# Kernel tuning notes

Hardware: AMD Instinct MI355X
Metric: run time of the kernel (lower is better)

## Reference

```python
import math
import jax, jax.numpy as jnp
import numpy as np

STRIDE = 8
IMG = 2048
NA = 9            # num anchors per cell (len(cfg['anchor_size']))
NC = 80           # num classes
TOPK = 1000
CONF = 0.05
NMS_T = 0.6
CTR_CLAMP = 32.0
EXP_CLAMP = math.log(1e8)            # DEFAULT_EXP_CLAMP
SCALE_CLAMP = math.log(1000.0 / 16)  # DEFAULT_SCALE_CLAMP


def setup_inputs() -> dict:
    key = jax.random.key(0)
    k1, k2, k3 = jax.random.split(key, 3)
    H = W = IMG // STRIDE  # 256
    obj_pred = jax.random.normal(k1, (1, NA, H, W), jnp.float32)
    cls_pred = jax.random.normal(k2, (1, NA * NC, H, W), jnp.float32)
    reg_pred = jax.random.normal(k3, (1, NA * 4, H, W), jnp.float32) * 0.5
    # generate_anchors: grid centers (+0.5)*stride, tiled anchor sizes -> [H*W*NA, 4] (cx,cy,w,h)
    ys, xs = jnp.meshgrid(jnp.arange(H), jnp.arange(W), indexing='ij')
    xy = (jnp.stack([xs, ys], -1).reshape(-1, 2).astype(jnp.float32) + 0.5) * STRIDE
    sizes = jnp.array([[32, 32], [64, 64], [128, 128], [32, 64], [64, 128],
                       [128, 256], [64, 32], [128, 64], [256, 128]], jnp.float32)
    anchor_boxes = jnp.concatenate(
        [jnp.repeat(xy[:, None, :], NA, axis=1),
         jnp.broadcast_to(sizes[None], (H * W, NA, 2))], axis=-1).reshape(-1, 4)
    return {"obj_pred": obj_pred, "cls_pred": cls_pred,
            "reg_pred": reg_pred, "anchor_boxes": anchor_boxes}


def _detect(obj_pred, cls_pred, reg_pred, anchor_boxes):
    B, _, H, W = obj_pred.shape
    obj = obj_pred.reshape(B, NA, 1, H, W)
    cls = cls_pred.reshape(B, NA, NC, H, W)
    # normalized_cls_pred = cls + obj - log(1 + exp(clamp(cls)) + exp(clamp(obj)))
    norm = cls + obj - jnp.log(1.0 + jnp.exp(jnp.minimum(cls, EXP_CLAMP))
                               + jnp.exp(jnp.minimum(obj, EXP_CLAMP)))
    norm = norm.transpose(0, 3, 4, 1, 2).reshape(B, -1, NC)[0]          # [M, NC]
    reg = reg_pred.reshape(B, NA, 4, H, W).transpose(0, 3, 4, 1, 2).reshape(B, -1, 4)[0]  # [M, 4]
    prob = jax.nn.sigmoid(norm)
    scores_all = prob.max(axis=-1)
    labels_all = prob.argmax(axis=-1)
    scores, idx = jax.lax.top_k(scores_all, TOPK)                        # descending
    labels = labels_all[idx]
    reg = reg[idx]
    anc = anchor_boxes[idx]
    # decode_boxes
    ctr_off = jnp.clip(reg[..., :2] * anc[..., 2:], -CTR_CLAMP, CTR_CLAMP)
    ctr = anc[..., :2] + ctr_off
    wh = anc[..., 2:] * jnp.exp(jnp.minimum(reg[..., 2:], SCALE_CLAMP))
    boxes = jnp.concatenate([ctr - 0.5 * wh, ctr + 0.5 * wh], axis=-1)
    boxes = jnp.clip(boxes / IMG, 0.0, 1.0)
    return scores, labels, boxes


def _nms_keep(scores, labels, boxes):
    # scores are sorted descending; per-class greedy NMS == class-masked global greedy NMS
    valid = scores >= CONF
    x1, y1, x2, y2 = boxes[:, 0], boxes[:, 1], boxes[:, 2], boxes[:, 3]
    areas = (x2 - x1) * (y2 - y1)
    xx1 = jnp.maximum(x1[:, None], x1[None, :])
    yy1 = jnp.maximum(y1[:, None], y1[None, :])
    xx2 = jnp.minimum(x2[:, None], x2[None, :])
    yy2 = jnp.minimum(y2[:, None], y2[None, :])
    inter = jnp.maximum(1e-28, xx2 - xx1) * jnp.maximum(1e-28, yy2 - yy1)
    iou = inter / (areas[:, None] + areas[None, :] - inter + 1e-14)      # [N, N]
    sup = (iou > NMS_T) & (labels[:, None] == labels[None, :])
    later = jnp.arange(TOPK)[None, :] > jnp.arange(TOPK)[:, None]

    def body(i, keep):
        row = sup[i] & later[i] & keep[i]   # i suppresses only if still kept
        return keep & ~row

    return jax.lax.fori_loop(0, TOPK, body, valid)


def reference(obj_pred, cls_pred, reg_pred, anchor_boxes):
    scores, labels, boxes = _detect(obj_pred, cls_pred, reg_pred, anchor_boxes)
    keep = _nms_keep(scores, labels, boxes)
    # fixed-shape outputs: detections sorted by score with a keep mask
    return scores, labels, boxes, keep
```

## Files before the change

kernel.cpp:

```cpp
#include <hip/hip_runtime.h>
#include <stdint.h>

#define NA 9
#define NC 80
#define NTOT 589824
#define NT4  147456
#define TOPK 1000
#define CONF 0.05f
#define NMS_T 0.6
#define CTR_CLAMP 32.0
#define IMGF 2048.0
#define SCALE_CLAMP 4.135166556742356

#define BITS_OFF   0u
#define LABELS_OFF 2359296u
#define HIST_OFF   4718592u
#define CNT_OFF    4784128u
#define BARC_OFF   4784384u
#define FLAG_OFF   4792576u
#define INITF_OFF  4800768u
#define CAND_OFF   4802816u
#define BOXES_OFF  4835584u
#define LABS_OFF   4851584u
#define SUPB_OFF   4855584u

#define NBLK 512
#define SPIN_CAP 200000
#define INIT_MAGIC 0x9E3779B97F4A7C15ull

__device__ __forceinline__ void stg32(unsigned* p, unsigned v) {
  __hip_atomic_store(p, v, __ATOMIC_RELAXED, __HIP_MEMORY_SCOPE_AGENT);
}
__device__ __forceinline__ unsigned ldg32(const unsigned* p) {
  return __hip_atomic_load((unsigned*)p, __ATOMIC_RELAXED, __HIP_MEMORY_SCOPE_AGENT);
}
__device__ __forceinline__ void stg64(unsigned long long* p, unsigned long long v) {
  __hip_atomic_store(p, v, __ATOMIC_RELAXED, __HIP_MEMORY_SCOPE_AGENT);
}
__device__ __forceinline__ unsigned long long ldg64(const unsigned long long* p) {
  return __hip_atomic_load((unsigned long long*)p, __ATOMIC_RELAXED,
                           __HIP_MEMORY_SCOPE_AGENT);
}

__device__ __forceinline__ unsigned* lslot(unsigned* base, int idx) {
  return (unsigned*)((char*)base + (size_t)idx * 256u);
}

__device__ __forceinline__ void barrier_sync(unsigned* cnts, unsigned* flags,
                                             int b, int bid, unsigned target,
                                             bool i_arrive) {
  __syncthreads();
  if (threadIdx.x == 0) {
    if (i_arrive)
      __hip_atomic_fetch_add(lslot(cnts, b * 8 + (bid & 7)), 1u, __ATOMIC_RELAXED,
                             __HIP_MEMORY_SCOPE_AGENT);
    if (bid == 0) {
      for (int it = 0; it < SPIN_CAP; it++) {
        unsigned s = 0;
#pragma unroll
        for (int i = 0; i < 8; i++)
          s += __hip_atomic_load(lslot(cnts, b * 8 + i), __ATOMIC_RELAXED,
                                 __HIP_MEMORY_SCOPE_AGENT);
        if (s >= target) break;
        __builtin_amdgcn_s_sleep(2);
      }
#pragma unroll
      for (int i = 0; i < 8; i++)
        __hip_atomic_store(lslot(flags, b * 8 + i), 1u, __ATOMIC_RELAXED,
                           __HIP_MEMORY_SCOPE_AGENT);
    } else {
      for (int it = 0; it < SPIN_CAP; it++) {
        if (__hip_atomic_load(lslot(flags, b * 8 + (bid & 7)), __ATOMIC_RELAXED,
                              __HIP_MEMORY_SCOPE_AGENT) != 0u)
          break;
        __builtin_amdgcn_s_sleep(2);
      }
    }
  }
  __syncthreads();
  asm volatile("" ::: "memory");
}

__device__ __forceinline__ float cexpf(float x) {
#pragma clang fp contract(off)
  float m = floorf(__builtin_fmaf(x, 1.44269504088896341f, 0.5f));
  float r = __builtin_fmaf(m, -0.693359375f, x);
  r = __builtin_fmaf(m, 2.12194440e-4f, r);
  float r2 = r * r;
  float y = 1.9875691500E-4f;
  y = __builtin_fmaf(y, r, 1.3981999507E-3f);
  y = __builtin_fmaf(y, r, 8.3334519073E-3f);
  y = __builtin_fmaf(y, r, 4.1665795894E-2f);
  y = __builtin_fmaf(y, r, 1.6666665459E-1f);
  y = __builtin_fmaf(y, r, 5.0000001201E-1f);
  y = __builtin_fmaf(y, r2, r) + 1.0f;
  return ldexpf(y, (int)m);
}

__device__ __forceinline__ float clogf_(float xin) {
#pragma clang fp contract(off)
  unsigned b = __float_as_uint(xin);
  int e = (int)(b >> 23) - 126;
  float m = __uint_as_float((b & 0x007FFFFFu) | 0x3F000000u);
  if (m < 0.707106781186547524f) { e -= 1; m = m + m; }
  float x = m - 1.0f;
  float z = x * x;
  float y = 7.0376836292E-2f;
  y = __builtin_fmaf(y, x, -1.1514610310E-1f);
  y = __builtin_fmaf(y, x, 1.1676998740E-1f);
  y = __builtin_fmaf(y, x, -1.2420140846E-1f);
  y = __builtin_fmaf(y, x, 1.4249322787E-1f);
  y = __builtin_fmaf(y, x, -1.6668057665E-1f);
  y = __builtin_fmaf(y, x, 2.0000714765E-1f);
  y = __builtin_fmaf(y, x, -2.4999993993E-1f);
  y = __builtin_fmaf(y, x, 3.3333331174E-1f);
  y = y * x * z;
  float ef = (float)e;
  y = __builtin_fmaf(ef, -2.12194440e-4f, y);
  y = __builtin_fmaf(-0.5f, z, y);
  float res = x + y;
  res = __builtin_fmaf(ef, 0.693359375f, res);
  return res;
}

__device__ __forceinline__ unsigned long long shflxor64(unsigned long long v, int m) {
  unsigned lo = __shfl_xor((unsigned)v, m, 64);
  unsigned hi = __shfl_xor((unsigned)(v >> 32), m, 64);
  return ((unsigned long long)hi << 32) | lo;
}

__global__ __launch_bounds__(256) void k_fused(
    const float4* __restrict__ obj4, const float4* __restrict__ cls4,
    unsigned* __restrict__ bits_all, int* __restrict__ labels_all,
    unsigned* __restrict__ hist, const float* __restrict__ reg_pred,
    const float* __restrict__ anchors, unsigned* __restrict__ cand_cnt,
    unsigned* __restrict__ barc, unsigned* __restrict__ flags,
    unsigned* __restrict__ initf, unsigned long long* __restrict__ cand,
    float* __restrict__ out, float* __restrict__ boxes_s,
    int* __restrict__ labels_s, unsigned long long* __restrict__ supB) {
  int tid = threadIdx.x;
  int bid = blockIdx.x;

  __shared__ __align__(16) unsigned lh[16384];

  for (int i = tid; i < 16384; i += 256) lh[i] = 0u;
  if (bid == 0) {
    for (int i = tid; i < 16384; i += 256) stg32(&hist[i], 0u);
    if (tid == 0) stg32(cand_cnt, 0u);
    if (tid < 32) {
      stg32(lslot(barc, tid), 0u);
      stg32(lslot(flags, tid), 0u);
    }
  }
  __syncthreads();
  if (bid == 0 && tid < 8)
    stg64((unsigned long long*)lslot(initf, tid), INIT_MAGIC);

  {
#pragma clang fp contract(off)
    for (unsigned t4 = (unsigned)bid * 256u + (unsigned)tid; t4 < (unsigned)NT4;
         t4 += (unsigned)(NBLK * 256)) {
      int a = (int)(t4 >> 14);
      int rem = (int)(t4 & 16383u);
      float4 ov = obj4[t4];
      float ob[4] = {ov.x, ov.y, ov.z, ov.w};
      float best[4] = {-1e30f, -1e30f, -1e30f, -1e30f};
      int bc[4] = {0, 0, 0, 0};
      const float4* cp = cls4 + a * 80 * 16384 + rem;
#pragma unroll 8
      for (int c = 0; c < 80; c++) {
        float4 cv = cp[c * 16384];
        float cl[4] = {cv.x, cv.y, cv.z, cv.w};
#pragma unroll
        for (int k = 0; k < 4; k++) {
          if (cl[k] > best[k]) { best[k] = cl[k]; bc[k] = c; }
        }
      }
      unsigned bv[4];
#pragma unroll
      for (int k = 0; k < 4; k++) {
        float c = best[k], o = ob[k];
        float ec = cexpf(c);
        float eo = cexpf(o);
        float L = clogf_((1.0f + ec) + eo);
        float nrm = (c + o) - L;
        float p = 1.0f / (1.0f + cexpf(-nrm));
        bv[k] = __float_as_uint(p);
        atomicAdd(&lh[bv[k] >> 16], 1u);
      }
      unsigned po = (unsigned)(a * 65536 + rem * 4);
      stg64((unsigned long long*)&bits_all[po],
            (unsigned long long)bv[0] | ((unsigned long long)bv[1] << 32));
      stg64((unsigned long long*)&bits_all[po + 2],
            (unsigned long long)bv[2] | ((unsigned long long)bv[3] << 32));
      stg64((unsigned long long*)&labels_all[po],
            (unsigned long long)(unsigned)bc[0] |
                ((unsigned long long)(unsigned)bc[1] << 32));
      stg64((unsigned long long*)&labels_all[po + 2],
            (unsigned long long)(unsigned)bc[2] |
                ((unsigned long long)(unsigned)bc[3] << 32));
    }
  }
  __syncthreads();
  if (tid == 0) {
    for (int it = 0; it < SPIN_CAP; it++) {
      if (ldg64((unsigned long long*)lslot(initf, bid & 7)) == INIT_MAGIC) break;
      __builtin_amdgcn_s_sleep(2);
    }
  }
  __syncthreads();
  for (int b = tid; b < 16384; b += 256) {
    unsigned v = lh[b];
    if (v) atomicAdd(&hist[b], v);
  }
  barrier_sync(barc, flags, 0, bid, NBLK, true);

  unsigned cB;
  {
    unsigned base = (unsigned)tid * 64u;
    unsigned s = 0;
#pragma unroll 8
    for (int b = 0; b < 64; b++) s += hist[base + b];
    unsigned v = s;
    lh[tid] = v;
    __syncthreads();
    for (int off = 1; off < 256; off <<= 1) {
      unsigned add = (tid + off < 256) ? lh[tid + off] : 0u;
      __syncthreads();
      v += add;
      lh[tid] = v;
      __syncthreads();
    }
    unsigned nxt = (tid < 255) ? lh[tid + 1] : 0u;
    if (v >= TOPK && nxt < TOPK) { lh[260] = (unsigned)tid; lh[261] = nxt; }
    __syncthreads();
    unsigned C = lh[260];
    unsigned above = lh[261];
    if (tid < 64) {
      unsigned h = hist[C * 64u + (unsigned)tid];
      unsigned acc = h;
      for (int off = 1; off < 64; off <<= 1) {
        unsigned o = __shfl_down(acc, off, 64);
        if (tid + off < 64) acc += o;
      }
      acc += above;
      if (acc >= TOPK && (tid == 63 || (acc - h) < TOPK))
        lh[262] = C * 64u + (unsigned)tid;
    }
    __syncthreads();
    cB = lh[262];
  }

  for (unsigned t = (unsigned)bid * 256u + (unsigned)tid; t < (unsigned)NTOT;
       t += (unsigned)(NBLK * 256)) {
    unsigned bits = bits_all[t];
    bool win = (bits >> 16) >= cB;
    unsigned long long m = __ballot(win);
    if (m != 0ull) {
      int lane = tid & 63;
      int leader = __ffsll((long long)m) - 1;
      unsigned base2 = 0;
      if (lane == leader) base2 = atomicAdd(cand_cnt, (unsigned)__popcll(m));
      base2 = __shfl(base2, leader, 64);
      if (win) {
        unsigned a = t >> 16;
        unsigned hw = t & 65535u;
        unsigned j = hw * 9u + a;
        unsigned pos = base2 + (unsigned)__popcll(m & ((1ull << lane) - 1ull));
        if (pos < 4096u)
          stg64(&cand[pos], ((unsigned long long)bits << 20) |
                                (unsigned long long)(0xFFFFFu - j));
      }
    }
  }
  barrier_sync(barc, flags, 1, bid, NBLK, true);

  if (bid < 16) {
    unsigned long long* s_key = (unsigned long long*)lh;
    int c = bid * 256 + tid;
    unsigned M = ldg32(cand_cnt);
    if (M > 4096u) M = 4096u;
    unsigned long long mykey = (c < (int)M) ? ldg64(&cand[c]) : 0ull;
    unsigned rank = 0;
    int ntile = (int)((M + 255u) >> 8);
    for (int tile = 0; tile < ntile; tile++) {
      __syncthreads();
      int src = tile * 256 + tid;
      s_key[tid] = (src < (int)M) ? ldg64(&cand[src]) : 0ull;
      __syncthreads();
#pragma unroll 8
      for (int q = 0; q < 256; q++) rank += (s_key[q] > mykey) ? 1u : 0u;
    }
    if (c < (int)M && rank < TOPK) {
      int r = (int)rank;
      unsigned j = 0xFFFFFu - (unsigned)(mykey & 0xFFFFFull);
      unsigned hw = j / 9u;
      unsigned a = j - hw * 9u;
      int lab = labels_all[a * 65536u + hw];
      unsigned base = a * 4u * 65536u + hw;
      double r0 = (double)reg_pred[base];
      double r1 = (double)reg_pred[base + 65536u];
      double r2 = (double)reg_pred[base + 131072u];
      double r3 = (double)reg_pred[base + 196608u];
      double ax = (double)anchors[j * 4u + 0], ay = (double)anchors[j * 4u + 1];
      double aw = (double)anchors[j * 4u + 2], ah = (double)anchors[j * 4u + 3];
      double ox = fmin(fmax(r0 * aw, -CTR_CLAMP), CTR_CLAMP);
      double oy = fmin(fmax(r1 * ah, -CTR_CLAMP), CTR_CLAMP);
      double cx = ax + ox, cy = ay + oy;
      double ww = aw * exp(fmin(r2, SCALE_CLAMP));
      double hh = ah * exp(fmin(r3, SCALE_CLAMP));
      float x1 = (float)fmin(fmax((cx - 0.5 * ww) * (1.0 / IMGF), 0.0), 1.0);
      float y1 = (float)fmin(fmax((cy - 0.5 * hh) * (1.0 / IMGF), 0.0), 1.0);
      float x2 = (float)fmin(fmax((cx + 0.5 * ww) * (1.0 / IMGF), 0.0), 1.0);
      float y2 = (float)fmin(fmax((cy + 0.5 * hh) * (1.0 / IMGF), 0.0), 1.0);
      out[1000 + r] = (float)lab;
      out[2000 + 4 * r + 0] = x1;
      out[2000 + 4 * r + 1] = y1;
      out[2000 + 4 * r + 2] = x2;
      out[2000 + 4 * r + 3] = y2;
      stg32((unsigned*)&out[r], (unsigned)(mykey >> 20));
      stg32((unsigned*)&boxes_s[4 * r + 0], __float_as_uint(x1));
      stg32((unsigned*)&boxes_s[4 * r + 1], __float_as_uint(y1));
      stg32((unsigned*)&boxes_s[4 * r + 2], __float_as_uint(x2));
      stg32((unsigned*)&boxes_s[4 * r + 3], __float_as_uint(y2));
      stg32((unsigned*)&labels_s[r], (unsigned)lab);
    }
  }
  barrier_sync(barc, flags, 2, bid, 16, bid < 16);

  {
    float* s_bx = (float*)lh;
    int* s_lb = (int*)((char*)lh + 16000);
    for (int t = tid; t < 4000; t += 256)
      s_bx[t] = __uint_as_float(ldg32((const unsigned*)&boxes_s[t]));
    for (int t = tid; t < 1000; t += 256)
      s_lb[t] = (int)ldg32((const unsigned*)&labels_s[t]);
    __syncthreads();
    for (int half = 0; half < 2; half++) {
      int i = bid + half * NBLK;
      if (i < TOPK) {
        double ix1 = (double)s_bx[4 * i], iy1 = (double)s_bx[4 * i + 1];
        double ix2 = (double)s_bx[4 * i + 2], iy2 = (double)s_bx[4 * i + 3];
        double ia = (ix2 - ix1) * (iy2 - iy1);
        int il = s_lb[i];
        for (int rep = 0; rep < 4; rep++) {
          int j = rep * 256 + tid;
          bool s = false;
          if (j < TOPK && j > i && s_lb[j] == il) {
            double jx1 = (double)s_bx[4 * j], jy1 = (double)s_bx[4 * j + 1];
            double jx2 = (double)s_bx[4 * j + 2], jy2 = (double)s_bx[4 * j + 3];
            double xx1 = fmax(ix1, jx1), yy1 = fmax(iy1, jy1);
            double xx2 = fmin(ix2, jx2), yy2 = fmin(iy2, jy2);
            double inter = fmax(1e-28, xx2 - xx1) * fmax(1e-28, yy2 - yy1);
            double ja = (jx2 - jx1) * (jy2 - jy1);
            double iou = inter / (ia + ja - inter + 1e-14);
            s = iou > NMS_T;
          }
          unsigned long long w = __ballot(s);
          if ((tid & 63) == 0)
            stg64(&supB[(rep * 4 + (tid >> 6)) * 1024 + i], w);
        }
      }
    }
  }
  __syncthreads();
  if (tid == 0)
    __hip_atomic_fetch_add(lslot(barc, 3 * 8 + (bid & 7)), 1u, __ATOMIC_RELAXED,
                           __HIP_MEMORY_SCOPE_AGENT);
  if (bid != 0) return;
  if (tid == 0) {
    for (int it = 0; it < SPIN_CAP; it++) {
      unsigned s = 0;
#pragma unroll
      for (int i = 0; i < 8; i++)
        s += __hip_atomic_load(lslot(barc, 3 * 8 + i), __ATOMIC_RELAXED,
                               __HIP_MEMORY_SCOPE_AGENT);
      if (s >= NBLK) break;
      __builtin_amdgcn_s_sleep(2);
    }
  }
  __syncthreads();
  asm volatile("" ::: "memory");

  if (tid < 64) {
    int lane = tid;
    float* keep_out = out + 6000;
    unsigned long long inval[16];
#pragma unroll
    for (int m = 0; m < 16; m++) {
      int j = m * 64 + lane;
      bool bad = (j >= TOPK) ||
                 (__uint_as_float(ldg32((const unsigned*)&out[j])) < CONF);
      inval[m] = __ballot(bad);
    }
    unsigned long long kept[16];
#pragma unroll
    for (int b = 0; b < 16; b++) {
      unsigned long long acc = 0ull;
#pragma unroll
      for (int m = 0; m < b; m++) {
        unsigned long long r = ldg64(&supB[b * 1024 + m * 64 + lane]);
        if ((kept[m] >> lane) & 1ull) acc |= r;
      }
      if (b > 0) {
#pragma unroll
        for (int s = 1; s < 64; s <<= 1) acc |= shflxor64(acc, s);
      }
      unsigned alo = __builtin_amdgcn_readfirstlane((unsigned)acc);
      unsigned ahi = __builtin_amdgcn_readfirstlane((unsigned)(acc >> 32));
      unsigned long long cur = inval[b] | (((unsigned long long)ahi << 32) | alo);
      unsigned long long diag = ldg64(&supB[b * 1024 + b * 64 + lane]);
      unsigned dlo = (unsigned)diag, dhi = (unsigned)(diag >> 32);
#pragma unroll 8
      for (int k = 0; k < 64; k++) {
        unsigned rlo = __builtin_amdgcn_readlane(dlo, k);
        unsigned rhi = __builtin_amdgcn_readlane(dhi, k);
        unsigned long long rk = ((unsigned long long)rhi << 32) | rlo;
        unsigned long long take = ((cur >> k) & 1ull) ? 0ull : rk;
        cur |= take;
      }
      kept[b] = ~cur;
    }
#pragma unroll
    for (int m = 0; m < 16; m++) {
      int j = m * 64 + lane;
      if (j < TOPK) keep_out[j] = ((kept[m] >> lane) & 1ull) ? 1.0f : 0.0f;
    }
  }
}

extern "C" void kernel_launch(void* const* d_in, const int* in_sizes, int n_in,
                              void* d_out, int out_size, void* d_ws, size_t ws_size,
                              hipStream_t stream) {
  const float* obj = (const float*)d_in[0];
  const float* cls = (const float*)d_in[1];
  const float* reg = (const float*)d_in[2];
  const float* anc = (const float*)d_in[3];
  float* out = (float*)d_out;
  char* ws = (char*)d_ws;

  const float4* obj4 = (const float4*)obj;
  const float4* cls4 = (const float4*)cls;
  unsigned* bits_all = (unsigned*)(ws + BITS_OFF);
  int* labels_all = (int*)(ws + LABELS_OFF);
  unsigned* hist = (unsigned*)(ws + HIST_OFF);
  unsigned* cand_cnt = (unsigned*)(ws + CNT_OFF);
  unsigned* barc = (unsigned*)(ws + BARC_OFF);
  unsigned* flags = (unsigned*)(ws + FLAG_OFF);
  unsigned* initf = (unsigned*)(ws + INITF_OFF);
  unsigned long long* cand = (unsigned long long*)(ws + CAND_OFF);
  float* boxes_s = (float*)(ws + BOXES_OFF);
  int* labels_s = (int*)(ws + LABS_OFF);
  unsigned long long* supB = (unsigned long long*)(ws + SUPB_OFF);

  void* kargs[] = {(void*)&obj4,     (void*)&cls4,     (void*)&bits_all,
                   (void*)&labels_all, (void*)&hist,   (void*)&reg,
                   (void*)&anc,      (void*)&cand_cnt, (void*)&barc,
                   (void*)&flags,    (void*)&initf,    (void*)&cand,
                   (void*)&out,      (void*)&boxes_s,  (void*)&labels_s,
                   (void*)&supB};
  hipLaunchCooperativeKernel((const void*)k_fused, dim3(NBLK), dim3(256), kargs, 0,
                             stream);
}
```

Baseline: 393.2 us.

## Keep per-anchor scores in registers across grid barrier; pack label into candidate key

Each thread now scores a fixed set of float4 groups (288 per block, with 8 lanes per wave taking one extra) and keeps the probabilities and labels in registers across the histogram barrier. Candidate selection then reads from registers instead of re-reading a global bits array. The class label is packed into the low bits of the 64-bit candidate key, which removes the global labels_all array and its gather during box decode. This cuts about 4.7 MB of global writes and reads, at the cost of more live registers and uneven work where a few lanes per wave do a second scoring pass.

```diff
diff --git a/kernel.cpp b/kernel.cpp
--- a/kernel.cpp
+++ b/kernel.cpp
@@ -12,8 +12,6 @@
 #define IMGF 2048.0
 #define SCALE_CLAMP 4.135166556742356
 
-#define BITS_OFF   0u
-#define LABELS_OFF 2359296u
 #define HIST_OFF   4718592u
 #define CNT_OFF    4784128u
 #define BARC_OFF   4784384u
@@ -25,6 +23,7 @@
 #define SUPB_OFF   4855584u
 
 #define NBLK 512
+#define PER_BLK 288
 #define SPIN_CAP 200000
 #define INIT_MAGIC 0x9E3779B97F4A7C15ull
 
@@ -129,9 +128,42 @@
   return ((unsigned long long)hi << 32) | lo;
 }
 
+__device__ __forceinline__ void score4(const float4* __restrict__ obj4,
+                                       const float4* __restrict__ cls4,
+                                       unsigned t4, unsigned bv[4], int bc[4],
+                                       unsigned* lh) {
+#pragma clang fp contract(off)
+  int a = (int)(t4 >> 14);
+  int rem = (int)(t4 & 16383u);
+  float4 ov = obj4[t4];
+  float ob[4] = {ov.x, ov.y, ov.z, ov.w};
+  float best[4] = {-1e30f, -1e30f, -1e30f, -1e30f};
+  bc[0] = bc[1] = bc[2] = bc[3] = 0;
+  const float4* cp = cls4 + a * 80 * 16384 + rem;
+#pragma unroll 8
+  for (int c = 0; c < 80; c++) {
+    float4 cv = cp[c * 16384];
+    float cl[4] = {cv.x, cv.y, cv.z, cv.w};
+#pragma unroll
+    for (int k = 0; k < 4; k++) {
+      if (cl[k] > best[k]) { best[k] = cl[k]; bc[k] = c; }
+    }
+  }
+#pragma unroll
+  for (int k = 0; k < 4; k++) {
+    float c = best[k], o = ob[k];
+    float ec = cexpf(c);
+    float eo = cexpf(o);
+    float L = clogf_((1.0f + ec) + eo);
+    float nrm = (c + o) - L;
+    float p = 1.0f / (1.0f + cexpf(-nrm));
+    bv[k] = __float_as_uint(p);
+    atomicAdd(&lh[bv[k] >> 16], 1u);
+  }
+}
+
 __global__ __launch_bounds__(256) void k_fused(
     const float4* __restrict__ obj4, const float4* __restrict__ cls4,
-    unsigned* __restrict__ bits_all, int* __restrict__ labels_all,
     unsigned* __restrict__ hist, const float* __restrict__ reg_pred,
     const float* __restrict__ anchors, unsigned* __restrict__ cand_cnt,
     unsigned* __restrict__ barc, unsigned* __restrict__ flags,
@@ -156,51 +188,15 @@
   if (bid == 0 && tid < 8)
     stg64((unsigned long long*)lslot(initf, tid), INIT_MAGIC);
 
-  {
-#pragma clang fp contract(off)
-    for (unsigned t4 = (unsigned)bid * 256u + (unsigned)tid; t4 < (unsigned)NT4;
-         t4 += (unsigned)(NBLK * 256)) {
-      int a = (int)(t4 >> 14);
-      int rem = (int)(t4 & 16383u);
-      float4 ov = obj4[t4];
-      float ob[4] = {ov.x, ov.y, ov.z, ov.w};
-      float best[4] = {-1e30f, -1e30f, -1e30f, -1e30f};
-      int bc[4] = {0, 0, 0, 0};
-      const float4* cp = cls4 + a * 80 * 16384 + rem;
-#pragma unroll 8
-      for (int c = 0; c < 80; c++) {
-        float4 cv = cp[c * 16384];
-        float cl[4] = {cv.x, cv.y, cv.z, cv.w};
-#pragma unroll
-        for (int k = 0; k < 4; k++) {
-          if (cl[k] > best[k]) { best[k] = cl[k]; bc[k] = c; }
-        }
-      }
-      unsigned bv[4];
-#pragma unroll
-      for (int k = 0; k < 4; k++) {
-        float c = best[k], o = ob[k];
-        float ec = cexpf(c);
-        float eo = cexpf(o);
-        float L = clogf_((1.0f + ec) + eo);
-        float nrm = (c + o) - L;
-        float p = 1.0f / (1.0f + cexpf(-nrm));
-        bv[k] = __float_as_uint(p);
-        atomicAdd(&lh[bv[k] >> 16], 1u);
-      }
-      unsigned po = (unsigned)(a * 65536 + rem * 4);
-      stg64((unsigned long long*)&bits_all[po],
-            (unsigned long long)bv[0] | ((unsigned long long)bv[1] << 32));
-      stg64((unsigned long long*)&bits_all[po + 2],
-            (unsigned long long)bv[2] | ((unsigned long long)bv[3] << 32));
-      stg64((unsigned long long*)&labels_all[po],
-            (unsigned long long)(unsigned)bc[0] |
-                ((unsigned long long)(unsigned)bc[1] << 32));
-      stg64((unsigned long long*)&labels_all[po + 2],
-            (unsigned long long)(unsigned)bc[2] |
-                ((unsigned long long)(unsigned)bc[3] << 32));
-    }
-  }
+  int lane = tid & 63, wv = tid >> 6;
+  unsigned t4a = (unsigned)bid * PER_BLK + (unsigned)tid;
+  unsigned t4b = (unsigned)bid * PER_BLK + 256u + (unsigned)(wv * 8 + lane);
+  bool has1 = (lane < 8);
+  unsigned bv0[4], bv1[4] = {0, 0, 0, 0};
+  int bc0[4], bc1[4] = {0, 0, 0, 0};
+  score4(obj4, cls4, t4a, bv0, bc0, lh);
+  if (has1) score4(obj4, cls4, t4b, bv1, bc1, lh);
+
   __syncthreads();
   if (tid == 0) {
     for (int it = 0; it < SPIN_CAP; it++) {
@@ -251,25 +247,47 @@
     cB = lh[262];
   }
 
-  for (unsigned t = (unsigned)bid * 256u + (unsigned)tid; t < (unsigned)NTOT;
-       t += (unsigned)(NBLK * 256)) {
-    unsigned bits = bits_all[t];
-    bool win = (bits >> 16) >= cB;
-    unsigned long long m = __ballot(win);
-    if (m != 0ull) {
-      int lane = tid & 63;
-      int leader = __ffsll((long long)m) - 1;
-      unsigned base2 = 0;
-      if (lane == leader) base2 = atomicAdd(cand_cnt, (unsigned)__popcll(m));
-      base2 = __shfl(base2, leader, 64);
-      if (win) {
-        unsigned a = t >> 16;
-        unsigned hw = t & 65535u;
-        unsigned j = hw * 9u + a;
-        unsigned pos = base2 + (unsigned)__popcll(m & ((1ull << lane) - 1ull));
-        if (pos < 4096u)
-          stg64(&cand[pos], ((unsigned long long)bits << 20) |
-                                (unsigned long long)(0xFFFFFu - j));
+  {
+#pragma unroll
+    for (int k = 0; k < 4; k++) {
+      bool win = (bv0[k] >> 16) >= cB;
+      unsigned long long m = __ballot(win);
+      if (m != 0ull) {
+        int leader = __ffsll((long long)m) - 1;
+        unsigned base2 = 0;
+        if (lane == leader) base2 = atomicAdd(cand_cnt, (unsigned)__popcll(m));
+        base2 = __shfl(base2, leader, 64);
+        if (win) {
+          unsigned w = 4u * t4a + (unsigned)k;
+          unsigned a = w >> 16, hw = w & 65535u;
+          unsigned j = hw * 9u + a;
+          unsigned pos = base2 + (unsigned)__popcll(m & ((1ull << lane) - 1ull));
+          if (pos < 4096u)
+            stg64(&cand[pos], ((unsigned long long)bv0[k] << 27) |
+                                  ((unsigned long long)(0xFFFFFu - j) << 7) |
+                                  (unsigned long long)(unsigned)bc0[k]);
+        }
+      }
+    }
+#pragma unroll
+    for (int k = 0; k < 4; k++) {
+      bool win = has1 && ((bv1[k] >> 16) >= cB);
+      unsigned long long m = __ballot(win);
+      if (m != 0ull) {
+        int leader = __ffsll((long long)m) - 1;
+        unsigned base2 = 0;
+        if (lane == leader) base2 = atomicAdd(cand_cnt, (unsigned)__popcll(m));
+        base2 = __shfl(base2, leader, 64);
+        if (win) {
+          unsigned w = 4u * t4b + (unsigned)k;
+          unsigned a = w >> 16, hw = w & 65535u;
+          unsigned j = hw * 9u + a;
+          unsigned pos = base2 + (unsigned)__popcll(m & ((1ull << lane) - 1ull));
+          if (pos < 4096u)
+            stg64(&cand[pos], ((unsigned long long)bv1[k] << 27) |
+                                  ((unsigned long long)(0xFFFFFu - j) << 7) |
+                                  (unsigned long long)(unsigned)bc1[k]);
+        }
       }
     }
   }
@@ -293,10 +311,10 @@
     }
     if (c < (int)M && rank < TOPK) {
       int r = (int)rank;
-      unsigned j = 0xFFFFFu - (unsigned)(mykey & 0xFFFFFull);
+      int lab = (int)(mykey & 0x7Full);
+      unsigned j = 0xFFFFFu - (unsigned)((mykey >> 7) & 0xFFFFFull);
       unsigned hw = j / 9u;
       unsigned a = j - hw * 9u;
-      int lab = labels_all[a * 65536u + hw];
       unsigned base = a * 4u * 65536u + hw;
       double r0 = (double)reg_pred[base];
       double r1 = (double)reg_pred[base + 65536u];
@@ -318,7 +336,7 @@
       out[2000 + 4 * r + 1] = y1;
       out[2000 + 4 * r + 2] = x2;
       out[2000 + 4 * r + 3] = y2;
-      stg32((unsigned*)&out[r], (unsigned)(mykey >> 20));
+      stg32((unsigned*)&out[r], (unsigned)(mykey >> 27));
       stg32((unsigned*)&boxes_s[4 * r + 0], __float_as_uint(x1));
       stg32((unsigned*)&boxes_s[4 * r + 1], __float_as_uint(y1));
       stg32((unsigned*)&boxes_s[4 * r + 2], __float_as_uint(x2));
@@ -383,7 +401,6 @@
   asm volatile("" ::: "memory");
 
   if (tid < 64) {
-    int lane = tid;
     float* keep_out = out + 6000;
     unsigned long long inval[16];
 #pragma unroll
@@ -441,8 +458,6 @@
 
   const float4* obj4 = (const float4*)obj;
   const float4* cls4 = (const float4*)cls;
-  unsigned* bits_all = (unsigned*)(ws + BITS_OFF);
-  int* labels_all = (int*)(ws + LABELS_OFF);
   unsigned* hist = (unsigned*)(ws + HIST_OFF);
   unsigned* cand_cnt = (unsigned*)(ws + CNT_OFF);
   unsigned* barc = (unsigned*)(ws + BARC_OFF);
@@ -453,12 +468,11 @@
   int* labels_s = (int*)(ws + LABS_OFF);
   unsigned long long* supB = (unsigned long long*)(ws + SUPB_OFF);
 
-  void* kargs[] = {(void*)&obj4,     (void*)&cls4,     (void*)&bits_all,
-                   (void*)&labels_all, (void*)&hist,   (void*)&reg,
-                   (void*)&anc,      (void*)&cand_cnt, (void*)&barc,
-                   (void*)&flags,    (void*)&initf,    (void*)&cand,
-                   (void*)&out,      (void*)&boxes_s,  (void*)&labels_s,
-                   (void*)&supB};
+  void* kargs[] = {(void*)&obj4,  (void*)&cls4,     (void*)&hist,
+                   (void*)&reg,   (void*)&anc,      (void*)&cand_cnt,
+                   (void*)&barc,  (void*)&flags,    (void*)&initf,
+                   (void*)&cand,  (void*)&out,      (void*)&boxes_s,
+                   (void*)&labels_s, (void*)&supB};
   hipLaunchCooperativeKernel((const void*)k_fused, dim3(NBLK), dim3(256), kargs, 0,
                              stream);
 }
```

After: 400.3 us. No clear change (+1.8%).
